# Kernel tuning notes

Hardware: AMD Instinct MI355X
Metric: run time of the kernel (lower is better)

Reference implementation:

```python
import jax, jax.numpy as jnp
import numpy as np
import math

B = 2; SEQ = 4096; D_MODEL = 768; D_STATE = 128; D_CONV = 4; EXPAND = 2; HEAD_DIM = 64
D_INNER = EXPAND * D_MODEL; D_SSM = D_INNER; NH = D_SSM // HEAD_DIM  # 24 heads
CONV_DIM = D_SSM + 2 * D_STATE; CHUNK = 256
D_IN_PROJ = 2 * D_INNER + 2 * D_STATE + NH


def causal_conv1d(x, w, b):
    # x: [B, C, L]; w: [C, W] depthwise kernel; left-pad for causality; silu activation
    W = w.shape[-1]; L = x.shape[-1]
    xp = jnp.pad(x, ((0, 0), (0, 0), (W - 1, 0)))
    y = b[None, :, None] + sum(xp[:, :, k:k + L] * w[None, :, k, None] for k in range(W))
    return jax.nn.silu(y)


def segsum(a):
    # a: [..., S] -> [..., S, S]; entry (i,j) = sum_{k=j+1..i} a_k for i>=j, -inf above diag
    S = a.shape[-1]
    cs = jnp.cumsum(a, -1)
    d = cs[..., :, None] - cs[..., None, :]
    mask = jnp.tril(jnp.ones((S, S), bool))
    return jnp.where(mask, d, -jnp.inf)


def ssd_chunk_scan(x, dt, A, Bm, Cm, Dp, chunk):
    # Mamba2 SSD chunked selective scan. x:[b,l,h,p] dt:[b,l,h] A:[h] Bm,Cm:[b,l,n] Dp:[h]
    b, l, h, p = x.shape; n = Bm.shape[-1]; nc = l // chunk
    xc = x.reshape(b, nc, chunk, h, p)
    Bc = Bm.reshape(b, nc, chunk, n)
    Cc = Cm.reshape(b, nc, chunk, n)
    dtc = dt.reshape(b, nc, chunk, h)
    a = jnp.transpose(A[None, None, None, :] * dtc, (0, 3, 1, 2))  # [b,h,c,s]
    Acs = jnp.cumsum(a, -1)
    Lm = jnp.exp(segsum(a))  # [b,h,c,s,s] lower-triangular decay
    # intra-chunk (diagonal block) outputs
    Ydiag = jnp.einsum('bcsn,bczn,bhcsz,bczh,bczhp->bcshp', Cc, Bc, Lm, dtc, xc)
    # per-chunk end states
    decay_states = jnp.exp(Acs[..., -1:] - Acs)  # [b,h,c,s]
    states = jnp.einsum('bczn,bhcz,bczh,bczhp->bchpn', Bc, decay_states, dtc, xc)
    # inter-chunk recurrence over nc chunks (small) via scan
    decay_chunk = jnp.exp(Acs[..., -1])  # [b,h,c]
    def step(hcar, inp):
        dcy, st = inp
        return dcy[..., None, None] * hcar + st, hcar  # emit state entering chunk
    _, prev = jax.lax.scan(step, jnp.zeros_like(states[:, 0]),
                           (jnp.moveaxis(decay_chunk, -1, 0), jnp.moveaxis(states, 1, 0)))
    prev = jnp.moveaxis(prev, 0, 1)  # [b,c,h,p,n]
    Yoff = jnp.einsum('bcsn,bchpn,bhcs->bcshp', Cc, prev, jnp.exp(Acs))
    return (Ydiag + Yoff).reshape(b, l, h, p) + Dp[None, None, :, None] * x


def _forward(u, time_diff, W_in, b_in, conv_w, conv_b, tconv1_w, tconv1_b,
             tconv2_w, tconv2_b, mlp_w1, mlp_b1, mlp_w2, mlp_b2, gate_w, gate_b,
             ln_w, ln_b, A_log, dt_bias, Dp, norm_w, W_out, b_out):
    silu = jax.nn.silu
    zxbcdt = u @ W_in.T + b_in  # [B,L,d_in_proj], d_mlp=0
    z = zxbcdt[..., :D_SSM]
    xBC = zxbcdt[..., D_SSM:D_SSM + CONV_DIM]
    dt = zxbcdt[..., D_SSM + CONV_DIM:]  # [B,L,H]
    A = -jnp.exp(A_log)
    xBC = jnp.transpose(causal_conv1d(jnp.transpose(xBC, (0, 2, 1)), conv_w, conv_b), (0, 2, 1))
    # time-gated dt path (time_diff: [B,H,L])
    ts = silu(time_diff @ mlp_w1.T + mlp_b1) @ mlp_w2.T + mlp_b2
    tdt = ts * time_diff
    tdt = causal_conv1d(tdt, tconv1_w, tconv1_b)
    tdt = causal_conv1d(tdt, tconv2_w, tconv2_b)  # [B,H,L]
    final_dt = dt * jnp.transpose(tdt, (0, 2, 1))
    x = xBC[..., :D_SSM]
    Bm = xBC[..., D_SSM:D_SSM + D_STATE]
    Cm = xBC[..., D_SSM + D_STATE:]
    dt_sp = jax.nn.softplus(final_dt + dt_bias)
    xh = x.reshape(x.shape[0], x.shape[1], NH, HEAD_DIM)
    y = ssd_chunk_scan(xh, dt_sp, A, Bm, Cm, Dp, CHUNK).reshape(x.shape[0], x.shape[1], D_SSM)
    # gated RMSNorm (norm_before_gate=False): gate first, then normalize
    yg = y * silu(z)
    y = yg * jax.lax.rsqrt(jnp.mean(yg * yg, -1, keepdims=True) + 1e-12) * norm_w
    out = y @ W_out.T + b_out
    # time residual gate + LayerNorm over seq_len
    tg = jax.nn.sigmoid(time_diff @ gate_w.T + gate_b)  # [B,H,1]
    tmix = tg * time_diff + (1.0 - tg) * tdt
    mu = jnp.mean(tmix, -1, keepdims=True)
    var = jnp.mean((tmix - mu) ** 2, -1, keepdims=True)
    time_out = (tmix - mu) * jax.lax.rsqrt(var + 1e-12) * ln_w + ln_b
    return out, time_out


def setup_inputs():
    key = jax.random.key(0)
    ks = jax.random.split(key, 16)
    def nrm(k, shape, scale=0.02):
        return jax.random.normal(k, shape, jnp.float32) * scale
    dtv = jnp.exp(jax.random.uniform(ks[10], (NH,), jnp.float32) * (math.log(0.1) - math.log(0.001)) + math.log(0.001))
    dtv = jnp.clip(dtv, 1e-4)
    dt_bias = dtv + jnp.log(-jnp.expm1(-dtv))
    A_log = jnp.log(jax.random.uniform(ks[11], (NH,), jnp.float32, 1.0, 16.0))
    return dict(
        u=jax.random.normal(ks[0], (B, SEQ, D_MODEL), jnp.float32),
        time_diff=jax.random.uniform(ks[1], (B, NH, SEQ), jnp.float32),
        W_in=nrm(ks[2], (D_IN_PROJ, D_MODEL)), b_in=jnp.zeros((D_IN_PROJ,), jnp.float32),
        conv_w=nrm(ks[3], (CONV_DIM, D_CONV), 0.2), conv_b=jnp.zeros((CONV_DIM,), jnp.float32),
        tconv1_w=nrm(ks[4], (NH, D_CONV), 0.2), tconv1_b=jnp.zeros((NH,), jnp.float32),
        tconv2_w=nrm(ks[5], (NH, D_CONV), 0.2), tconv2_b=jnp.zeros((NH,), jnp.float32),
        mlp_w1=nrm(ks[6], (SEQ, SEQ)), mlp_b1=jnp.zeros((SEQ,), jnp.float32),
        mlp_w2=nrm(ks[7], (SEQ, SEQ)), mlp_b2=jnp.zeros((SEQ,), jnp.float32),
        gate_w=nrm(ks[8], (1, SEQ)), gate_b=jnp.zeros((1,), jnp.float32),
        ln_w=jnp.ones((SEQ,), jnp.float32), ln_b=jnp.zeros((SEQ,), jnp.float32),
        A_log=A_log, dt_bias=dt_bias, Dp=jnp.ones((NH,), jnp.float32),
        norm_w=jnp.ones((D_SSM,), jnp.float32),
        W_out=nrm(ks[9], (D_MODEL, D_INNER)), b_out=jnp.zeros((D_MODEL,), jnp.float32),
    )


def reference(u, time_diff, W_in, b_in, conv_w, conv_b, tconv1_w, tconv1_b,
              tconv2_w, tconv2_b, mlp_w1, mlp_b1, mlp_w2, mlp_b2, gate_w, gate_b,
              ln_w, ln_b, A_log, dt_bias, Dp, norm_w, W_out, b_out):
    return _forward(u, time_diff, W_in, b_in, conv_w, conv_b, tconv1_w, tconv1_b,
                    tconv2_w, tconv2_b, mlp_w1, mlp_b1, mlp_w2, mlp_b2, gate_w, gate_b,
                    ln_w, ln_b, A_log, dt_bias, Dp, norm_w, W_out, b_out)
```

## Files before the change

### kernel.cpp

```cpp
#include <hip/hip_runtime.h>
#include <math.h>

#define BB 2
#define SEQ 4096
#define DMODEL 768
#define DSTATE 128
#define NHH 24
#define HDIM 64
#define DSSM 1536
#define CDIM 1792
#define CHK 256
#define NC 16
#define DPROJ 3352
#define MR (BB*SEQ)
#define KSPLIT 32
#define XSTR 1920
#define CT 16
#define SXS 270
#define STS 134

typedef __attribute__((ext_vector_type(8))) short bf16x8;
typedef __attribute__((ext_vector_type(8))) unsigned short u16x8;
typedef __attribute__((ext_vector_type(4))) float f32x4;

__device__ __forceinline__ float siluf(float x) { return x / (1.0f + expf(-x)); }

__device__ __forceinline__ unsigned short f2bf(float f) {
    unsigned u = __float_as_uint(f);
    unsigned r = (u + 0x7fffu + ((u >> 16) & 1u)) >> 16;
    return (unsigned short)r;
}

__device__ __forceinline__ float bf2f(unsigned short u) {
    return __uint_as_float(((unsigned)u) << 16);
}

__device__ __forceinline__ float4 bf2f4(ushort4 v) {
    float4 o;
    o.x = bf2f(v.x); o.y = bf2f(v.y); o.z = bf2f(v.z); o.w = bf2f(v.w);
    return o;
}

__device__ __forceinline__ bf16x8 pack8(float4 a, float4 b) {
    u16x8 r;
    r[0] = f2bf(a.x); r[1] = f2bf(a.y); r[2] = f2bf(a.z); r[3] = f2bf(a.w);
    r[4] = f2bf(b.x); r[5] = f2bf(b.y); r[6] = f2bf(b.z); r[7] = f2bf(b.w);
    return *(bf16x8*)&r;
}

__device__ __forceinline__ void gload_lds16(const void* g, void* l) {
    __builtin_amdgcn_global_load_lds((const __attribute__((address_space(1))) unsigned int*)g,
                                     (__attribute__((address_space(3))) unsigned int*)l, 16, 0, 0);
}

__global__ __launch_bounds__(256) void cvt3_k(
    const float* __restrict__ in0, unsigned short* __restrict__ out0, int nb0, int nv0,
    const float* __restrict__ in1, unsigned short* __restrict__ out1, int nb1, int nv1,
    const float* __restrict__ in2, unsigned short* __restrict__ out2, int nb2, int nv2)
{
    int b = blockIdx.x;
    const float* in; unsigned short* out; int nvalid; int base;
    if (b < nb0) { in = in0; out = out0; nvalid = nv0; base = b; }
    else if (b < nb0 + nb1) { in = in1; out = out1; nvalid = nv1; base = b - nb0; }
    else { in = in2; out = out2; nvalid = nv2; base = b - nb0 - nb1; }
    int i = (base * 256 + threadIdx.x) * 4;
    ushort4 o;
    if (i + 3 < nvalid) {
        float4 v = *(const float4*)&in[i];
        o.x = f2bf(v.x); o.y = f2bf(v.y); o.z = f2bf(v.z); o.w = f2bf(v.w);
    } else {
        o.x = (i + 0 < nvalid) ? f2bf(in[i + 0]) : 0;
        o.y = (i + 1 < nvalid) ? f2bf(in[i + 1]) : 0;
        o.z = (i + 2 < nvalid) ? f2bf(in[i + 2]) : 0;
        o.w = (i + 3 < nvalid) ? f2bf(in[i + 3]) : 0;
    }
    *(ushort4*)&out[i] = o;
}

__global__ __launch_bounds__(256) void gemm_dual_skinny(
    const unsigned short* __restrict__ A,
    const unsigned short* __restrict__ B1, const float* __restrict__ bias1,
    unsigned short* __restrict__ C1, int N1, int NT1, int nbias1, int NWG1,
    const unsigned short* __restrict__ B2, const float* __restrict__ bias2,
    unsigned short* __restrict__ C2, int N2, int NT2, int nbias2,
    int K, int KT, int NWGD,
    const float* __restrict__ skA, const float* __restrict__ skB,
    float* __restrict__ skPart, int skN, int skK)
{
    __shared__ unsigned short SMEM[24576];
    const int tid = threadIdx.x;
    const int w = tid >> 6, l = tid & 63;
    const int lr = l & 15, lk = l >> 4;
    int nwg = gridDim.x, bid = blockIdx.x;
    int wg = (nwg & 7) ? bid : ((bid & 7) * (nwg >> 3) + (bid >> 3));
    if (wg >= NWGD) {
        int t = wg - NWGD;
        int nb = t & 31, kb = t >> 5;
        const int n0s = nb * 128;
        const int KS = skK / KSPLIT;
        const int k0 = kb * KS;
        const int nw0 = n0s + w * 32;
        f32x4 sacc[3][2] = {};
        for (int kt = 0; kt < KS; kt += 32) {
            int kk = k0 + kt + lk * 8;
            bf16x8 af[3], bfr[2];
#pragma unroll
            for (int mi = 0; mi < 3; ++mi) {
                const float* ap = &skA[(size_t)(mi * 16 + lr) * skK + kk];
                af[mi] = pack8(*(const float4*)ap, *(const float4*)(ap + 4));
            }
#pragma unroll
            for (int nf = 0; nf < 2; ++nf) {
                const float* bp = &skB[(size_t)(nw0 + nf * 16 + lr) * skK + kk];
                bfr[nf] = pack8(*(const float4*)bp, *(const float4*)(bp + 4));
            }
#pragma unroll
            for (int mi = 0; mi < 3; ++mi)
#pragma unroll
                for (int nf = 0; nf < 2; ++nf)
                    sacc[mi][nf] = __builtin_amdgcn_mfma_f32_16x16x32_bf16(af[mi], bfr[nf], sacc[mi][nf], 0, 0, 0);
        }
        float* pb = skPart + (size_t)kb * 48 * skN;
#pragma unroll
        for (int mi = 0; mi < 3; ++mi)
#pragma unroll
            for (int r = 0; r < 4; ++r)
#pragma unroll
                for (int nf = 0; nf < 2; ++nf)
                    pb[(size_t)(mi * 16 + lk * 4 + r) * skN + nw0 + nf * 16 + lr] = sacc[mi][nf][r];
        return;
    }
    const int wr = w >> 1, wc = w & 1;
    const int lkx = lk ^ ((lr >> 1) & 3);
    const unsigned short* B;
    const float* bias;
    unsigned short* C;
    int N, NT, nbias;
    if (wg < NWG1) { B = B1; bias = bias1; C = C1; N = N1; NT = NT1; nbias = nbias1; }
    else { wg -= NWG1; B = B2; bias = bias2; C = C2; N = N2; NT = NT2; nbias = nbias2; }
    const int m0 = (wg / NT) * 128, n0 = (wg % NT) * 128;
    f32x4 acc[4][4] = {};
    const int i16 = w * 64 + l;
    const int row0 = i16 >> 2, sl = i16 & 3;
    const int slx = sl ^ ((row0 >> 1) & 3);
    const size_t ga0 = (size_t)(m0 + row0) * K + slx * 8;
    const size_t ga1 = (size_t)(m0 + row0 + 64) * K + slx * 8;
    const size_t gb0 = (size_t)(n0 + row0) * K + slx * 8;
    const size_t gb1 = (size_t)(n0 + row0 + 64) * K + slx * 8;
    const int lo0 = (w * 64) * 8;
    const int lo1 = (256 + w * 64) * 8;

#define STAGE(bb, kt) { int ko = (kt) * 32; int bs = (bb) * 8192;            \
      gload_lds16(A + ga0 + ko, &SMEM[bs + lo0]);                            \
      gload_lds16(A + ga1 + ko, &SMEM[bs + lo1]);                            \
      gload_lds16(B + gb0 + ko, &SMEM[bs + 4096 + lo0]);                     \
      gload_lds16(B + gb1 + ko, &SMEM[bs + 4096 + lo1]); }

    STAGE(0, 0);
    STAGE(1, 1);
    for (int kt = 0; kt < KT; ++kt) {
        if (kt + 1 < KT) {
            asm volatile("s_waitcnt vmcnt(4)" ::: "memory");
        } else {
            asm volatile("s_waitcnt vmcnt(0)" ::: "memory");
        }
        __builtin_amdgcn_s_barrier();
        if (kt + 2 < KT) STAGE((kt + 2) % 3, kt + 2);
        int bs = (kt % 3) * 8192;
        bf16x8 af[4], bg[4];
#pragma unroll
        for (int mi = 0; mi < 4; ++mi)
            af[mi] = *(const bf16x8*)&SMEM[bs + (wr * 64 + mi * 16 + lr) * 32 + lkx * 8];
#pragma unroll
        for (int nj = 0; nj < 4; ++nj)
            bg[nj] = *(const bf16x8*)&SMEM[bs + 4096 + (wc * 64 + nj * 16 + lr) * 32 + lkx * 8];
#pragma unroll
        for (int mi = 0; mi < 4; ++mi)
#pragma unroll
            for (int nj = 0; nj < 4; ++nj)
                acc[mi][nj] = __builtin_amdgcn_mfma_f32_16x16x32_bf16(af[mi], bg[nj], acc[mi][nj], 0, 0, 0);
    }
#undef STAGE
    {
        unsigned short* CL = SMEM;
#pragma unroll
        for (int half = 0; half < 2; ++half) {
            __syncthreads();
            if (wr == half) {
#pragma unroll
                for (int nj = 0; nj < 4; ++nj) {
                    int col = n0 + wc * 64 + nj * 16 + lr;
                    float bz = (col < nbias) ? bias[col] : 0.f;
                    int cl = wc * 64 + nj * 16 + lr;
#pragma unroll
                    for (int mi = 0; mi < 4; ++mi)
#pragma unroll
                        for (int r = 0; r < 4; ++r)
                            CL[(mi * 16 + lk * 4 + r) * 136 + cl] = f2bf(acc[mi][nj][r] + bz);
                }
            }
            __syncthreads();
            for (int i = tid; i < 1024; i += 256) {
                int rr = i >> 4, c8 = (i & 15) * 8;
                int m = m0 + half * 64 + rr;
                *(u16x8*)&C[(size_t)m * N + n0 + c8] = *(const u16x8*)&CL[rr * 136 + c8];
            }
        }
    }
}

__global__ __launch_bounds__(256) void conv_skinny2_k(const unsigned short* __restrict__ xbc,
    const float* __restrict__ cw, const float* __restrict__ cb,
    unsigned short* __restrict__ out,
    const float* __restrict__ skA, const float* __restrict__ skB,
    float* __restrict__ skPart, int skN, int skK, int NWGC)
{
    int bid = blockIdx.x;
    int tid = threadIdx.x;
    if (bid >= NWGC) {
        int t = bid - NWGC;
        int nb = t & 31, kb = t >> 5;
        const int n0s = nb * 128;
        const int KS = skK / KSPLIT;
        const int k0 = kb * KS;
        const int w = tid >> 6, l = tid & 63;
        const int lr = l & 15, lk = l >> 4;
        const int nw0 = n0s + w * 32;
        f32x4 sacc[3][2] = {};
        for (int kt = 0; kt < KS; kt += 32) {
            int kk = k0 + kt + lk * 8;
            bf16x8 af[3], bfr[2];
#pragma unroll
            for (int mi = 0; mi < 3; ++mi) {
                const float* ap = &skA[(size_t)(mi * 16 + lr) * skK + kk];
                af[mi] = pack8(*(const float4*)ap, *(const float4*)(ap + 4));
            }
#pragma unroll
            for (int nf = 0; nf < 2; ++nf) {
                const float* bp = &skB[(size_t)(nw0 + nf * 16 + lr) * skK + kk];
                bfr[nf] = pack8(*(const float4*)bp, *(const float4*)(bp + 4));
            }
#pragma unroll
            for (int mi = 0; mi < 3; ++mi)
#pragma unroll
                for (int nf = 0; nf < 2; ++nf)
                    sacc[mi][nf] = __builtin_amdgcn_mfma_f32_16x16x32_bf16(af[mi], bfr[nf], sacc[mi][nf], 0, 0, 0);
        }
        float* pb = skPart + (size_t)kb * 48 * skN;
#pragma unroll
        for (int mi = 0; mi < 3; ++mi)
#pragma unroll
            for (int r = 0; r < 4; ++r)
#pragma unroll
                for (int nf = 0; nf < 2; ++nf)
                    pb[(size_t)(mi * 16 + lk * 4 + r) * skN + nw0 + nf * 16 + lr] = sacc[mi][nf][r];
        return;
    }
    int idx = bid * 256 + tid;
    int slot = idx % 448;
    int g = idx / 448;
    int c4 = slot * 4;
    int b = g / (SEQ / CT);
    int t0 = (g % (SEQ / CT)) * CT;
    size_t rb = (size_t)b * SEQ;
    float4 cw0 = *(const float4*)&cw[(c4 + 0) * 4];
    float4 cw1 = *(const float4*)&cw[(c4 + 1) * 4];
    float4 cw2 = *(const float4*)&cw[(c4 + 2) * 4];
    float4 cw3 = *(const float4*)&cw[(c4 + 3) * 4];
    float4 cbv = *(const float4*)&cb[c4];
    float4 zero = {0.f, 0.f, 0.f, 0.f};
    float4 w0, w1, w2;
    w0 = (t0 - 3 >= 0) ? bf2f4(*(const ushort4*)&xbc[(rb + t0 - 3) * XSTR + c4]) : zero;
    w1 = (t0 - 2 >= 0) ? bf2f4(*(const ushort4*)&xbc[(rb + t0 - 2) * XSTR + c4]) : zero;
    w2 = (t0 - 1 >= 0) ? bf2f4(*(const ushort4*)&xbc[(rb + t0 - 1) * XSTR + c4]) : zero;
#pragma unroll
    for (int i = 0; i < CT; ++i) {
        int t = t0 + i;
        float4 w3 = bf2f4(*(const ushort4*)&xbc[(rb + t) * XSTR + c4]);
        float a0 = cbv.x + w0.x * cw0.x + w1.x * cw0.y + w2.x * cw0.z + w3.x * cw0.w;
        float a1 = cbv.y + w0.y * cw1.x + w1.y * cw1.y + w2.y * cw1.z + w3.y * cw1.w;
        float a2 = cbv.z + w0.z * cw2.x + w1.z * cw2.y + w2.z * cw2.z + w3.z * cw2.w;
        float a3 = cbv.w + w0.w * cw3.x + w1.w * cw3.y + w2.w * cw3.z + w3.w * cw3.w;
        ushort4 o;
        o.x = f2bf(siluf(a0)); o.y = f2bf(siluf(a1));
        o.z = f2bf(siluf(a2)); o.w = f2bf(siluf(a3));
        *(ushort4*)&out[(rb + t) * CDIM + c4] = o;
        w0 = w1; w1 = w2; w2 = w3;
    }
}

__global__ __launch_bounds__(256) void reduce_part_k(const float* __restrict__ part,
    const float* __restrict__ bias, float* __restrict__ out, int N, int act)
{
    int idx = blockIdx.x * 256 + threadIdx.x;
    if (idx >= 48 * N) return;
    int n = idx % N;
    float s = bias[n];
#pragma unroll
    for (int kb = 0; kb < KSPLIT; ++kb) s += part[(size_t)kb * 48 * N + idx];
    if (act) s = siluf(s);
    out[idx] = s;
}

__global__ __launch_bounds__(256) void time_conv_k(const float* __restrict__ ts,
    const float* __restrict__ td, const float* __restrict__ w1, const float* __restrict__ b1,
    const float* __restrict__ w2, const float* __restrict__ b2, float* __restrict__ tdt)
{
    __shared__ float u0[SEQ];
    __shared__ float u1[SEQ];
    int row = blockIdx.x, h = row % NHH;
    const float* tsr = ts + (size_t)row * SEQ;
    const float* tdr = td + (size_t)row * SEQ;
    for (int i = threadIdx.x; i < SEQ; i += 256) u0[i] = tsr[i] * tdr[i];
    __syncthreads();
    float wa[4], wb[4];
#pragma unroll
    for (int k = 0; k < 4; ++k) { wa[k] = w1[h * 4 + k]; wb[k] = w2[h * 4 + k]; }
    float ba = b1[h], bbv = b2[h];
    for (int i = threadIdx.x; i < SEQ; i += 256) {
        float acc = ba;
#pragma unroll
        for (int k = 0; k < 4; ++k) { int tt = i + k - 3; if (tt >= 0) acc = fmaf(u0[tt], wa[k], acc); }
        u1[i] = siluf(acc);
    }
    __syncthreads();
    for (int i = threadIdx.x; i < SEQ; i += 256) {
        float acc = bbv;
#pragma unroll
        for (int k = 0; k < 4; ++k) { int tt = i + k - 3; if (tt >= 0) acc = fmaf(u1[tt], wb[k], acc); }
        tdt[(size_t)row * SEQ + i] = siluf(acc);
    }
}

__global__ __launch_bounds__(256) void dtsp_cum_k(const unsigned short* __restrict__ r1,
    const float* __restrict__ tdt, const float* __restrict__ dt_bias,
    const float* __restrict__ A_log, float* __restrict__ dtp, float* __restrict__ acs)
{
    __shared__ float wsum[4];
    int blk = blockIdx.x;
    int c = blk % NC;
    int bh = blk / NC;
    int h = bh % NHH, b = bh / NHH;
    int tid = threadIdx.x;
    int s = c * CHK + tid;
    size_t base = (size_t)bh * SEQ + s;
    float x = bf2f(r1[((size_t)(b * SEQ + s)) * XSTR + CDIM + h]) * tdt[base] + dt_bias[h];
    float dt = (x > 20.0f) ? x : log1pf(expf(x));
    dtp[base] = dt;
    float Ah = -expf(A_log[h]);
    float v = Ah * dt;
    int ln = tid & 63;
#pragma unroll
    for (int off = 1; off < 64; off <<= 1) {
        float t = __shfl_up(v, off, 64);
        if (ln >= off) v += t;
    }
    if (ln == 63) wsum[tid >> 6] = v;
    __syncthreads();
    float add = 0.f;
    int wv = tid >> 6;
#pragma unroll
    for (int i = 0; i < 3; ++i)
        if (i < wv) add += wsum[i];
    acs[base] = v + add;
}

__global__ __launch_bounds__(256) void ssd_states_sraw_k(const unsigned short* __restrict__ xc,
    const float* __restrict__ dtp, const float* __restrict__ acs_g,
    float* __restrict__ st, unsigned short* __restrict__ sraw)
{
    __shared__ float s_coef[256];
    __shared__ unsigned short SXT[64 * STS];
    __shared__ unsigned short SBT[128 * STS];
    int bid = blockIdx.x;
    int blk = (gridDim.x & 7) ? bid : ((bid & 7) * (gridDim.x >> 3) + (bid >> 3));
    int tid = threadIdx.x;
    int w = tid >> 6, l = tid & 63;
    int lr = l & 15, lk = l >> 4;
    if (blk >= BB * NC * NHH) {
        int t = blk - BB * NC * NHH;
        int bc = t / 10, tile = t % 10;
        int rem = tile, st_i = 0;
        for (st_i = 0; ; ++st_i) { if (rem < st_i + 1) break; rem -= st_i + 1; }
        int zt = rem;
        int b = bc / NC, c = bc % NC;
        size_t rowbase = (size_t)b * SEQ + c * CHK;
        for (int i = tid; i < 64 * 32; i += 256) {
            int r = i >> 5, c4 = (i & 31) * 4;
            *(ushort4*)&SXT[r * STS + c4] = *(const ushort4*)&xc[(rowbase + st_i * 64 + r) * CDIM + DSSM + DSTATE + c4];
            *(ushort4*)&SBT[r * STS + c4] = *(const ushort4*)&xc[(rowbase + zt * 64 + r) * CDIM + DSSM + c4];
        }
        __syncthreads();
        f32x4 d[4] = {};
        __builtin_amdgcn_s_setprio(1);
#pragma unroll
        for (int kt = 0; kt < 4; ++kt) {
            bf16x8 av = *(const bf16x8*)&SXT[(w * 16 + lr) * STS + kt * 32 + lk * 8];
            bf16x8 bv[4];
#pragma unroll
            for (int nj = 0; nj < 4; ++nj)
                bv[nj] = *(const bf16x8*)&SBT[(nj * 16 + lr) * STS + kt * 32 + lk * 8];
#pragma unroll
            for (int nj = 0; nj < 4; ++nj)
                d[nj] = __builtin_amdgcn_mfma_f32_16x16x32_bf16(av, bv[nj], d[nj], 0, 0, 0);
        }
        __builtin_amdgcn_s_setprio(0);
        unsigned short* tp = sraw + (size_t)bc * 16 * 4096 + (size_t)(st_i * 4 + zt) * 4096;
#pragma unroll
        for (int nj = 0; nj < 4; ++nj)
#pragma unroll
            for (int r = 0; r < 4; ++r)
                tp[(w * 16 + lk * 4 + r) * 64 + nj * 16 + lr] = f2bf(d[nj][r]);
        return;
    }
    int h = blk % NHH, c = (blk / NHH) % NC, b = blk / (NHH * NC);
    size_t rowbase = (size_t)b * SEQ + c * CHK;
    size_t dbase = (size_t)(b * NHH + h) * SEQ + c * CHK;
    float alv = acs_g[dbase + 255];
    s_coef[tid] = expf(alv - acs_g[dbase + tid]) * dtp[dbase + tid];
    __syncthreads();
    f32x4 acc[4][2] = {};
    for (int z0 = 0; z0 < CHK; z0 += 128) {
        if (z0) __syncthreads();
        for (int i = tid; i < 128 * 8; i += 256) {
            int zz = i >> 3, p8 = (i & 7) * 8;
            float sc = s_coef[z0 + zz];
            u16x8 v = *(const u16x8*)&xc[(rowbase + z0 + zz) * CDIM + h * HDIM + p8];
#pragma unroll
            for (int e = 0; e < 8; ++e)
                SXT[(p8 + e) * STS + zz] = f2bf(bf2f(v[e]) * sc);
        }
        for (int i = tid; i < 128 * 16; i += 256) {
            int zz = i >> 4, n8 = (i & 15) * 8;
            u16x8 v = *(const u16x8*)&xc[(rowbase + z0 + zz) * CDIM + DSSM + n8];
#pragma unroll
            for (int e = 0; e < 8; ++e)
                SBT[(n8 + e) * STS + zz] = v[e];
        }
        __syncthreads();
#pragma unroll
        for (int kt = 0; kt < 4; ++kt) {
            bf16x8 av[4], bv[2];
#pragma unroll
            for (int mi = 0; mi < 4; ++mi)
                av[mi] = *(const bf16x8*)&SXT[(mi * 16 + lr) * STS + kt * 32 + lk * 8];
#pragma unroll
            for (int nj = 0; nj < 2; ++nj)
                bv[nj] = *(const bf16x8*)&SBT[(w * 32 + nj * 16 + lr) * STS + kt * 32 + lk * 8];
#pragma unroll
            for (int mi = 0; mi < 4; ++mi)
#pragma unroll
                for (int nj = 0; nj < 2; ++nj)
                    acc[mi][nj] = __builtin_amdgcn_mfma_f32_16x16x32_bf16(av[mi], bv[nj], acc[mi][nj], 0, 0, 0);
        }
    }
    size_t base = (size_t)blk * (HDIM * DSTATE);
#pragma unroll
    for (int mi = 0; mi < 4; ++mi)
#pragma unroll
        for (int r = 0; r < 4; ++r) {
            int p = mi * 16 + lk * 4 + r;
#pragma unroll
            for (int nj = 0; nj < 2; ++nj)
                st[base + p * DSTATE + w * 32 + nj * 16 + lr] = acc[mi][nj][r];
        }
}

__global__ __launch_bounds__(256) void ssd_scan_k(const float* __restrict__ st,
    const float* __restrict__ acs_g, unsigned short* __restrict__ pv16)
{
    int b = blockIdx.x / NHH, h = blockIdx.x % NHH;
    int tid = threadIdx.x;
    float carry[32];
#pragma unroll
    for (int j = 0; j < 32; ++j) carry[j] = 0.f;
    for (int c = 0; c < NC; ++c) {
        int bch = (b * NC + c) * NHH + h;
        size_t base = (size_t)bch * (HDIM * DSTATE);
        float dcy = expf(acs_g[(size_t)(b * NHH + h) * SEQ + c * CHK + 255]);
#pragma unroll
        for (int j = 0; j < 32; ++j) {
            pv16[base + tid + j * 256] = f2bf(carry[j]);
            carry[j] = fmaf(dcy, carry[j], st[base + tid + j * 256]);
        }
    }
}

__global__ __launch_bounds__(256) void ssd_y2_k(const unsigned short* __restrict__ xc,
    const float* __restrict__ dtp, const float* __restrict__ acs_g,
    const unsigned short* __restrict__ sraw, const unsigned short* __restrict__ pv16,
    const float* __restrict__ Dp, unsigned short* __restrict__ Ybf)
{
    __shared__ unsigned short SXT[32 * SXS];
    int bid = blockIdx.x;
    int blk2 = (gridDim.x & 7) ? bid : ((bid & 7) * (gridDim.x >> 3) + (bid >> 3));
    int half = blk2 & 1;
    int blk = blk2 >> 1;
    int h = blk % NHH;
    int c = (blk / NHH) % NC;
    int b = blk / (NHH * NC);
    int tid = threadIdx.x;
    int w = tid >> 6, l = tid & 63;
    int lr = l & 15, lk = l >> 4;
    int pbase = half * 32;
    size_t rowbase = (size_t)b * SEQ + c * CHK;
    size_t dbase = (size_t)(b * NHH + h) * SEQ + c * CHK;
    for (int i = tid; i < 256 * 4; i += 256) {
        int z = i >> 2, p8 = (i & 3) * 8;
        float az0q = acs_g[dbase + (z & 192)];
        float e = az0q - acs_g[dbase + z];
        if (e > 60.f) e = 60.f;
        float sc = expf(e) * dtp[dbase + z];
        u16x8 v = *(const u16x8*)&xc[(rowbase + z) * CDIM + h * HDIM + pbase + p8];
#pragma unroll
        for (int e2 = 0; e2 < 8; ++e2)
            SXT[(p8 + e2) * SXS + z] = f2bf(bf2f(v[e2]) * sc);
    }
    float az0w = acs_g[dbase + w * 64];
    float esw[4][4];
#pragma unroll
    for (int mi = 0; mi < 4; ++mi)
#pragma unroll
        for (int r = 0; r < 4; ++r)
            esw[mi][r] = expf(acs_g[dbase + w * 64 + mi * 16 + lk * 4 + r] - az0w);
    __syncthreads();

    const unsigned short* tbase = sraw + (size_t)(b * NC + c) * 16 * 4096;
    const unsigned short* pvbase = pv16 + (size_t)blk * (HDIM * DSTATE);
    f32x4 acc[4][2] = {};
    for (int zt = 0; zt < w; ++zt) {
        const unsigned short* tp = tbase + (size_t)(w * 4 + zt) * 4096;
        f32x4 tmp[4][2] = {};
        __builtin_amdgcn_s_setprio(1);
#pragma unroll
        for (int kt = 0; kt < 2; ++kt) {
            bf16x8 av[4], bv[2];
#pragma unroll
            for (int mi = 0; mi < 4; ++mi)
                av[mi] = *(const bf16x8*)&tp[(mi * 16 + lr) * 64 + kt * 32 + lk * 8];
#pragma unroll
            for (int nj = 0; nj < 2; ++nj)
                bv[nj] = *(const bf16x8*)&SXT[(nj * 16 + lr) * SXS + zt * 64 + kt * 32 + lk * 8];
#pragma unroll
            for (int mi = 0; mi < 4; ++mi)
#pragma unroll
                for (int nj = 0; nj < 2; ++nj)
                    tmp[mi][nj] = __builtin_amdgcn_mfma_f32_16x16x32_bf16(av[mi], bv[nj], tmp[mi][nj], 0, 0, 0);
        }
        __builtin_amdgcn_s_setprio(0);
        float rho = expf(az0w - acs_g[dbase + zt * 64]);
#pragma unroll
        for (int mi = 0; mi < 4; ++mi)
#pragma unroll
            for (int r = 0; r < 4; ++r) {
                float es = esw[mi][r] * rho;
#pragma unroll
                for (int nj = 0; nj < 2; ++nj)
                    acc[mi][nj][r] += es * tmp[mi][nj][r];
            }
    }
    {
        const unsigned short* tp = tbase + (size_t)(w * 4 + w) * 4096;
        f32x4 tmp[4][2] = {};
        __builtin_amdgcn_s_setprio(1);
#pragma unroll
        for (int kt = 0; kt < 2; ++kt) {
            bf16x8 av[4], bv[2];
#pragma unroll
            for (int mi = 0; mi < 4; ++mi) {
                av[mi] = *(const bf16x8*)&tp[(mi * 16 + lr) * 64 + kt * 32 + lk * 8];
                int zb = kt * 32 + lk * 8;
                int sl = mi * 16 + lr;
#pragma unroll
                for (int e = 0; e < 8; ++e)
                    if (zb + e > sl) av[mi][e] = 0;
            }
#pragma unroll
            for (int nj = 0; nj < 2; ++nj)
                bv[nj] = *(const bf16x8*)&SXT[(nj * 16 + lr) * SXS + w * 64 + kt * 32 + lk * 8];
#pragma unroll
            for (int mi = 0; mi < 4; ++mi)
#pragma unroll
                for (int nj = 0; nj < 2; ++nj)
                    tmp[mi][nj] = __builtin_amdgcn_mfma_f32_16x16x32_bf16(av[mi], bv[nj], tmp[mi][nj], 0, 0, 0);
        }
        __builtin_amdgcn_s_setprio(0);
#pragma unroll
        for (int mi = 0; mi < 4; ++mi)
#pragma unroll
            for (int r = 0; r < 4; ++r) {
                float es = esw[mi][r];
#pragma unroll
                for (int nj = 0; nj < 2; ++nj)
                    acc[mi][nj][r] += es * tmp[mi][nj][r];
            }
    }
    {
        f32x4 tmp[4][2] = {};
        __builtin_amdgcn_s_setprio(1);
#pragma unroll
        for (int kt = 0; kt < 4; ++kt) {
            bf16x8 av[4], bv[2];
#pragma unroll
            for (int mi = 0; mi < 4; ++mi)
                av[mi] = *(const bf16x8*)&xc[(rowbase + w * 64 + mi * 16 + lr) * CDIM + DSSM + DSTATE + kt * 32 + lk * 8];
#pragma unroll
            for (int nj = 0; nj < 2; ++nj)
                bv[nj] = *(const bf16x8*)&pvbase[(pbase + nj * 16 + lr) * DSTATE + kt * 32 + lk * 8];
#pragma unroll
            for (int mi = 0; mi < 4; ++mi)
#pragma unroll
                for (int nj = 0; nj < 2; ++nj)
                    tmp[mi][nj] = __builtin_amdgcn_mfma_f32_16x16x32_bf16(av[mi], bv[nj], tmp[mi][nj], 0, 0, 0);
        }
        __builtin_amdgcn_s_setprio(0);
        float eoff = expf(az0w);
#pragma unroll
        for (int mi = 0; mi < 4; ++mi)
#pragma unroll
            for (int r = 0; r < 4; ++r) {
                float es = esw[mi][r] * eoff;
#pragma unroll
                for (int nj = 0; nj < 2; ++nj)
                    acc[mi][nj][r] += es * tmp[mi][nj][r];
            }
    }
    float dph = Dp[h];
#pragma unroll
    for (int mi = 0; mi < 4; ++mi) {
#pragma unroll
        for (int r = 0; r < 4; ++r) {
            int s = w * 64 + mi * 16 + lk * 4 + r;
#pragma unroll
            for (int nj = 0; nj < 2; ++nj) {
                int p = pbase + nj * 16 + lr;
                float xv = bf2f(xc[(rowbase + s) * CDIM + h * HDIM + p]);
                Ybf[(rowbase + s) * DSSM + h * HDIM + p] = f2bf(acc[mi][nj][r] + dph * xv);
            }
        }
    }
}

__global__ __launch_bounds__(256) void rmsnorm_k(const unsigned short* __restrict__ Ybf_in,
    const unsigned short* __restrict__ zbf, const float* __restrict__ nw,
    unsigned short* __restrict__ Ybf_out)
{
    __shared__ float red[8];
    int row = blockIdx.x;
    const unsigned short* y = Ybf_in + (size_t)row * DSSM;
    const unsigned short* z = zbf + (size_t)row * DSSM;
    float v[6];
    float ss = 0.f;
#pragma unroll
    for (int k = 0; k < 6; ++k) {
        int i = threadIdx.x + k * 256;
        float g = bf2f(y[i]) * siluf(bf2f(z[i]));
        v[k] = g;
        ss = fmaf(g, g, ss);
    }
#pragma unroll
    for (int o = 32; o > 0; o >>= 1) ss += __shfl_down(ss, o, 64);
    int wv = threadIdx.x >> 6, ln = threadIdx.x & 63;
    if (ln == 0) red[wv] = ss;
    __syncthreads();
    float tot = red[0] + red[1] + red[2] + red[3];
    float sc = rsqrtf(tot / (float)DSSM + 1e-12f);
    unsigned short* yo = Ybf_out + (size_t)row * DSSM;
#pragma unroll
    for (int k = 0; k < 6; ++k) {
        int i = threadIdx.x + k * 256;
        yo[i] = f2bf(v[k] * sc * nw[i]);
    }
}

__global__ __launch_bounds__(256) void gemm_out_timeout_k(
    const unsigned short* __restrict__ A, const unsigned short* __restrict__ B,
    const float* __restrict__ bias, float* __restrict__ C, int N, int K, int KT, int NT, int NWGG,
    const float* __restrict__ td, const float* __restrict__ tdt,
    const float* __restrict__ gw, const float* __restrict__ gb,
    const float* __restrict__ lnw, const float* __restrict__ lnb, float* __restrict__ out2)
{
    __shared__ __align__(16) unsigned char SMEMRAW[49152];
    unsigned short* SMEM = (unsigned short*)SMEMRAW;
    const int tid = threadIdx.x;
    int nwg = gridDim.x, bid = blockIdx.x;
    int wg = (nwg & 7) ? bid : ((bid & 7) * (nwg >> 3) + (bid >> 3));
    if (wg >= NWGG) {
        float* tm = (float*)SMEMRAW;
        __shared__ float red[8];
        int row = wg - NWGG;
        const float* tdr = td + (size_t)row * SEQ;
        const float* tdtr = tdt + (size_t)row * SEQ;
        int wv = tid >> 6, ln = tid & 63;
        float part = 0.f;
        for (int i = tid; i < SEQ; i += 256) part = fmaf(tdr[i], gw[i], part);
#pragma unroll
        for (int o = 32; o > 0; o >>= 1) part += __shfl_down(part, o, 64);
        if (ln == 0) red[wv] = part;
        __syncthreads();
        float dot = red[0] + red[1] + red[2] + red[3];
        float tg = 1.f / (1.f + expf(-(dot + gb[0])));
        __syncthreads();
        float sum = 0.f;
        for (int i = tid; i < SEQ; i += 256) {
            float x = tg * tdr[i] + (1.f - tg) * tdtr[i];
            tm[i] = x;
            sum += x;
        }
#pragma unroll
        for (int o = 32; o > 0; o >>= 1) sum += __shfl_down(sum, o, 64);
        if (ln == 0) red[wv] = sum;
        __syncthreads();
        float mu = (red[0] + red[1] + red[2] + red[3]) / (float)SEQ;
        __syncthreads();
        float s2 = 0.f;
        for (int i = tid; i < SEQ; i += 256) { float d = tm[i] - mu; s2 = fmaf(d, d, s2); }
#pragma unroll
        for (int o = 32; o > 0; o >>= 1) s2 += __shfl_down(s2, o, 64);
        if (ln == 0) red[wv] = s2;
        __syncthreads();
        float var = (red[0] + red[1] + red[2] + red[3]) / (float)SEQ;
        float inv = rsqrtf(var + 1e-12f);
        for (int i = tid; i < SEQ; i += 256)
            out2[(size_t)row * SEQ + i] = (tm[i] - mu) * inv * lnw[i] + lnb[i];
        return;
    }
    const int w = tid >> 6, l = tid & 63;
    const int wr = w >> 1, wc = w & 1;
    const int lr = l & 15, lk = l >> 4;
    const int lkx = lk ^ ((lr >> 1) & 3);
    const int m0 = (wg / NT) * 128, n0 = (wg % NT) * 128;
    f32x4 acc[4][4] = {};
    const int i16 = w * 64 + l;
    const int row0 = i16 >> 2, sl = i16 & 3;
    const int slx = sl ^ ((row0 >> 1) & 3);
    const size_t ga0 = (size_t)(m0 + row0) * K + slx * 8;
    const size_t ga1 = (size_t)(m0 + row0 + 64) * K + slx * 8;
    const size_t gb0 = (size_t)(n0 + row0) * K + slx * 8;
    const size_t gb1 = (size_t)(n0 + row0 + 64) * K + slx * 8;
    const int lo0 = (w * 64) * 8;
    const int lo1 = (256 + w * 64) * 8;

#define STAGE3(bb, kt) { int ko = (kt) * 32; int bs = (bb) * 8192;           \
      gload_lds16(A + ga0 + ko, &SMEM[bs + lo0]);                            \
      gload_lds16(A + ga1 + ko, &SMEM[bs + lo1]);                            \
      gload_lds16(B + gb0 + ko, &SMEM[bs + 4096 + lo0]);                     \
      gload_lds16(B + gb1 + ko, &SMEM[bs + 4096 + lo1]); }

    STAGE3(0, 0);
    STAGE3(1, 1);
    for (int kt = 0; kt < KT; ++kt) {
        if (kt + 1 < KT) {
            asm volatile("s_waitcnt vmcnt(4)" ::: "memory");
        } else {
            asm volatile("s_waitcnt vmcnt(0)" ::: "memory");
        }
        __builtin_amdgcn_s_barrier();
        if (kt + 2 < KT) STAGE3((kt + 2) % 3, kt + 2);
        int bs = (kt % 3) * 8192;
        bf16x8 af[4], bg[4];
#pragma unroll
        for (int mi = 0; mi < 4; ++mi)
            af[mi] = *(const bf16x8*)&SMEM[bs + (wr * 64 + mi * 16 + lr) * 32 + lkx * 8];
#pragma unroll
        for (int nj = 0; nj < 4; ++nj)
            bg[nj] = *(const bf16x8*)&SMEM[bs + 4096 + (wc * 64 + nj * 16 + lr) * 32 + lkx * 8];
#pragma unroll
        for (int mi = 0; mi < 4; ++mi)
#pragma unroll
            for (int nj = 0; nj < 4; ++nj)
                acc[mi][nj] = __builtin_amdgcn_mfma_f32_16x16x32_bf16(af[mi], bg[nj], acc[mi][nj], 0, 0, 0);
    }
#undef STAGE3
#pragma unroll
    for (int nj = 0; nj < 4; ++nj) {
        int col = n0 + wc * 64 + nj * 16 + lr;
        float bz = bias[col];
#pragma unroll
        for (int mi = 0; mi < 4; ++mi) {
#pragma unroll
            for (int r = 0; r < 4; ++r) {
                int m = m0 + wr * 64 + mi * 16 + lk * 4 + r;
                C[(size_t)m * N + col] = acc[mi][nj][r] + bz;
            }
        }
    }
}

extern "C" void kernel_launch(void* const* d_in, const int* in_sizes, int n_in,
                              void* d_out, int out_size, void* d_ws, size_t ws_size,
                              hipStream_t stream)
{
    const float* u      = (const float*)d_in[0];
    const float* td     = (const float*)d_in[1];
    const float* W_in   = (const float*)d_in[2];
    const float* b_in   = (const float*)d_in[3];
    const float* conv_w = (const float*)d_in[4];
    const float* conv_b = (const float*)d_in[5];
    const float* t1w    = (const float*)d_in[6];
    const float* t1b    = (const float*)d_in[7];
    const float* t2w    = (const float*)d_in[8];
    const float* t2b    = (const float*)d_in[9];
    const float* m1w    = (const float*)d_in[10];
    const float* m1b    = (const float*)d_in[11];
    const float* m2w    = (const float*)d_in[12];
    const float* m2b    = (const float*)d_in[13];
    const float* gw     = (const float*)d_in[14];
    const float* gb     = (const float*)d_in[15];
    const float* lnw    = (const float*)d_in[16];
    const float* lnb    = (const float*)d_in[17];
    const float* A_log  = (const float*)d_in[18];
    const float* dt_bias= (const float*)d_in[19];
    const float* Dpv    = (const float*)d_in[20];
    const float* nw     = (const float*)d_in[21];
    const float* W_out  = (const float*)d_in[22];
    const float* b_out  = (const float*)d_in[23];
    float* out  = (float*)d_out;
    float* out2 = out + (size_t)MR * DMODEL;

    float* ws = (float*)d_ws;
    size_t o = 0;
    float* zbuf  = ws + o; o += (size_t)MR * DSSM;
    float* r1    = ws + o; o += (size_t)MR * DSSM;
    float* xcv   = ws + o; o += (size_t)MR * CDIM / 2;
    float* partb = ws + o; o += (size_t)KSPLIT * 48 * SEQ;
    float* hid   = ws + o; o += (size_t)BB * NHH * SEQ;
    float* tss   = ws + o; o += (size_t)BB * NHH * SEQ;
    float* tdt   = ws + o; o += (size_t)BB * NHH * SEQ;
    float* dtp   = ws + o; o += (size_t)MR * NHH;
    float* acs_g = ws + o; o += (size_t)MR * NHH;
    float* pvb   = ws + o; o += (size_t)BB * NC * NHH * HDIM * DSTATE;
    unsigned short* sraw = (unsigned short*)(ws + o); o += (size_t)BB * NC * 16 * 4096 / 2;
    unsigned short* r1b = (unsigned short*)r1;
    float* stb = r1;
    unsigned short* ybf16 = (unsigned short*)r1;
    unsigned short* xcv_bf = (unsigned short*)xcv;
    unsigned short* u_bf  = (unsigned short*)pvb;
    unsigned short* Wi_bf = (unsigned short*)(pvb + 3145728);
    unsigned short* pv16  = (unsigned short*)pvb;
    unsigned short* zbf   = (unsigned short*)zbuf;
    unsigned short* Y_bf  = (unsigned short*)xcv;
    unsigned short* Wo_bf = (unsigned short*)(zbuf + 6291456);

    dim3 blk(256);
    const int NWG1 = (XSTR / 128) * (MR / 128);
    const int NWGD = NWG1 + (DSSM / 128) * (MR / 128);
    const int NWGSK = (SEQ / 128) * KSPLIT;
    const int NWGC = 448 * (MR / CT) / 256;
    const int NB0 = MR * DMODEL / 1024;
    const int NB1 = 3456 * DMODEL / 1024;
    const int NB2 = DMODEL * DSSM / 1024;

    cvt3_k<<<dim3(NB0 + NB1 + NB2), blk, 0, stream>>>(
        u, u_bf, NB0, MR * DMODEL,
        W_in, Wi_bf, NB1, DPROJ * DMODEL,
        W_out, Wo_bf, NB2, DMODEL * DSSM);
    gemm_dual_skinny<<<dim3(NWGD + NWGSK), blk, 0, stream>>>(
        u_bf,
        Wi_bf + (size_t)DSSM * DMODEL, b_in + DSSM, r1b, XSTR, XSTR / 128, DPROJ - DSSM, NWG1,
        Wi_bf, b_in, zbf, DSSM, DSSM / 128, DSSM,
        DMODEL, DMODEL / 32, NWGD,
        td, m1w, partb, SEQ, SEQ);
    reduce_part_k<<<dim3((48 * SEQ + 255) / 256), blk, 0, stream>>>(partb, m1b, hid, SEQ, 1);
    conv_skinny2_k<<<dim3(NWGC + NWGSK), blk, 0, stream>>>(
        r1b, conv_w, conv_b, xcv_bf, hid, m2w, partb, SEQ, SEQ, NWGC);
    reduce_part_k<<<dim3((48 * SEQ + 255) / 256), blk, 0, stream>>>(partb, m2b, tss, SEQ, 0);
    time_conv_k<<<dim3(BB * NHH), blk, 0, stream>>>(tss, td, t1w, t1b, t2w, t2b, tdt);
    dtsp_cum_k<<<dim3(BB * NHH * NC), blk, 0, stream>>>(r1b, tdt, dt_bias, A_log, dtp, acs_g);
    ssd_states_sraw_k<<<dim3(BB * NC * NHH + BB * NC * 10), blk, 0, stream>>>(xcv_bf, dtp, acs_g, stb, sraw);
    ssd_scan_k<<<dim3(BB * NHH), blk, 0, stream>>>(stb, acs_g, pv16);
    ssd_y2_k<<<dim3(BB * NC * NHH * 2), blk, 0, stream>>>(xcv_bf, dtp, acs_g, sraw, pv16, Dpv, ybf16);
    rmsnorm_k<<<dim3(MR), blk, 0, stream>>>(ybf16, zbf, nw, Y_bf);
    gemm_out_timeout_k<<<dim3((DMODEL / 128) * (MR / 128) + BB * NHH), blk, 0, stream>>>(
        Y_bf, Wo_bf, b_out, out, DMODEL, DSSM, DSSM / 32, DMODEL / 128, (DMODEL / 128) * (MR / 128),
        td, tdt, gw, gb, lnw, lnb, out2);
}
```

Measured before the change: 321.0 us.

## Drop LDS staging in dual GEMM and split state scan across more blocks

The dual skinny GEMM no longer stages tiles through a triple-buffered LDS pipeline with async global-to-LDS loads. Each wave now reads its MFMA operands straight from global memory, and LDS shrinks to only the epilogue staging buffer. This should raise occupancy, but it loses cross-wave reuse and the software prefetch. Separately, the inter-chunk state scan gets eight times as many blocks, each carrying four state elements instead of 32, so the sequential scan has more parallelism.

```diff
diff --git a/kernel.cpp b/kernel.cpp
--- a/kernel.cpp
+++ b/kernel.cpp
@@ -87,7 +87,7 @@
     const float* __restrict__ skA, const float* __restrict__ skB,
     float* __restrict__ skPart, int skN, int skK)
 {
-    __shared__ unsigned short SMEM[24576];
+    __shared__ unsigned short CL[8704];
     const int tid = threadIdx.x;
     const int w = tid >> 6, l = tid & 63;
     const int lr = l & 15, lk = l >> 4;
@@ -131,7 +131,6 @@
         return;
     }
     const int wr = w >> 1, wc = w & 1;
-    const int lkx = lk ^ ((lr >> 1) & 3);
     const unsigned short* B;
     const float* bias;
     unsigned short* C;
@@ -140,49 +139,25 @@
     else { wg -= NWG1; B = B2; bias = bias2; C = C2; N = N2; NT = NT2; nbias = nbias2; }
     const int m0 = (wg / NT) * 128, n0 = (wg % NT) * 128;
     f32x4 acc[4][4] = {};
-    const int i16 = w * 64 + l;
-    const int row0 = i16 >> 2, sl = i16 & 3;
-    const int slx = sl ^ ((row0 >> 1) & 3);
-    const size_t ga0 = (size_t)(m0 + row0) * K + slx * 8;
-    const size_t ga1 = (size_t)(m0 + row0 + 64) * K + slx * 8;
-    const size_t gb0 = (size_t)(n0 + row0) * K + slx * 8;
-    const size_t gb1 = (size_t)(n0 + row0 + 64) * K + slx * 8;
-    const int lo0 = (w * 64) * 8;
-    const int lo1 = (256 + w * 64) * 8;
-
-#define STAGE(bb, kt) { int ko = (kt) * 32; int bs = (bb) * 8192;            \
-      gload_lds16(A + ga0 + ko, &SMEM[bs + lo0]);                            \
-      gload_lds16(A + ga1 + ko, &SMEM[bs + lo1]);                            \
-      gload_lds16(B + gb0 + ko, &SMEM[bs + 4096 + lo0]);                     \
-      gload_lds16(B + gb1 + ko, &SMEM[bs + 4096 + lo1]); }
-
-    STAGE(0, 0);
-    STAGE(1, 1);
+    const unsigned short* Ab = A + (size_t)(m0 + wr * 64 + lr) * K + lk * 8;
+    const unsigned short* Bb = B + (size_t)(n0 + wc * 64 + lr) * K + lk * 8;
+#pragma unroll 2
     for (int kt = 0; kt < KT; ++kt) {
-        if (kt + 1 < KT) {
-            asm volatile("s_waitcnt vmcnt(4)" ::: "memory");
-        } else {
-            asm volatile("s_waitcnt vmcnt(0)" ::: "memory");
-        }
-        __builtin_amdgcn_s_barrier();
-        if (kt + 2 < KT) STAGE((kt + 2) % 3, kt + 2);
-        int bs = (kt % 3) * 8192;
+        int ko = kt * 32;
         bf16x8 af[4], bg[4];
 #pragma unroll
         for (int mi = 0; mi < 4; ++mi)
-            af[mi] = *(const bf16x8*)&SMEM[bs + (wr * 64 + mi * 16 + lr) * 32 + lkx * 8];
+            af[mi] = *(const bf16x8*)&Ab[(size_t)(mi * 16) * K + ko];
 #pragma unroll
         for (int nj = 0; nj < 4; ++nj)
-            bg[nj] = *(const bf16x8*)&SMEM[bs + 4096 + (wc * 64 + nj * 16 + lr) * 32 + lkx * 8];
+            bg[nj] = *(const bf16x8*)&Bb[(size_t)(nj * 16) * K + ko];
 #pragma unroll
         for (int mi = 0; mi < 4; ++mi)
 #pragma unroll
             for (int nj = 0; nj < 4; ++nj)
                 acc[mi][nj] = __builtin_amdgcn_mfma_f32_16x16x32_bf16(af[mi], bg[nj], acc[mi][nj], 0, 0, 0);
     }
-#undef STAGE
     {
-        unsigned short* CL = SMEM;
 #pragma unroll
         for (int half = 0; half < 2; ++half) {
             __syncthreads();
@@ -469,19 +444,22 @@
 __global__ __launch_bounds__(256) void ssd_scan_k(const float* __restrict__ st,
     const float* __restrict__ acs_g, unsigned short* __restrict__ pv16)
 {
-    int b = blockIdx.x / NHH, h = blockIdx.x % NHH;
+    int bh = blockIdx.x >> 3;
+    int jg = blockIdx.x & 7;
+    int b = bh / NHH, h = bh % NHH;
     int tid = threadIdx.x;
-    float carry[32];
-#pragma unroll
-    for (int j = 0; j < 32; ++j) carry[j] = 0.f;
+    float carry[4];
+#pragma unroll
+    for (int j = 0; j < 4; ++j) carry[j] = 0.f;
     for (int c = 0; c < NC; ++c) {
         int bch = (b * NC + c) * NHH + h;
         size_t base = (size_t)bch * (HDIM * DSTATE);
         float dcy = expf(acs_g[(size_t)(b * NHH + h) * SEQ + c * CHK + 255]);
 #pragma unroll
-        for (int j = 0; j < 32; ++j) {
-            pv16[base + tid + j * 256] = f2bf(carry[j]);
-            carry[j] = fmaf(dcy, carry[j], st[base + tid + j * 256]);
+        for (int j = 0; j < 4; ++j) {
+            size_t idx = base + tid + (size_t)(jg * 4 + j) * 256;
+            pv16[idx] = f2bf(carry[j]);
+            carry[j] = fmaf(dcy, carry[j], st[idx]);
         }
     }
 }
@@ -868,7 +846,7 @@
     time_conv_k<<<dim3(BB * NHH), blk, 0, stream>>>(tss, td, t1w, t1b, t2w, t2b, tdt);
     dtsp_cum_k<<<dim3(BB * NHH * NC), blk, 0, stream>>>(r1b, tdt, dt_bias, A_log, dtp, acs_g);
     ssd_states_sraw_k<<<dim3(BB * NC * NHH + BB * NC * 10), blk, 0, stream>>>(xcv_bf, dtp, acs_g, stb, sraw);
-    ssd_scan_k<<<dim3(BB * NHH), blk, 0, stream>>>(stb, acs_g, pv16);
+    ssd_scan_k<<<dim3(BB * NHH * 8), blk, 0, stream>>>(stb, acs_g, pv16);
     ssd_y2_k<<<dim3(BB * NC * NHH * 2), blk, 0, stream>>>(xcv_bf, dtp, acs_g, sraw, pv16, Dpv, ybf16);
     rmsnorm_k<<<dim3(MR), blk, 0, stream>>>(ybf16, zbf, nw, Y_bf);
     gemm_out_timeout_k<<<dim3((DMODEL / 128) * (MR / 128) + BB * NHH), blk, 0, stream>>>(
```

New measurement: 450.4 us. 40.3% more time.
